# Kernel tuning notes

Measured on AMD Instinct MI355X. Metric: run time of the kernel, lower is better.

Reference implementation:

```python
import jax, jax.numpy as jnp
import numpy as np

NH, NKV, D = 16, 4, 64
E, NG, TKG, TOPK = 64, 8, 4, 8
RSF = 2.5
EPS = 1e-6
THETA = 10000.0

def rmsnorm(x, w, eps=EPS):
    v = jnp.mean(jnp.square(x.astype(jnp.float32)), axis=-1, keepdims=True)
    return (x * jax.lax.rsqrt(v + eps)).astype(x.dtype) * w

def rope_neox(x, pos):
    # x: [T, heads, D]; neox-style rotation over full head_dim
    d = x.shape[-1]
    inv = 1.0 / (THETA ** (jnp.arange(0, d, 2, dtype=jnp.float32) / d))
    f = pos.astype(jnp.float32)[:, None] * inv              # [T, d/2]
    cos = jnp.cos(f)[:, None, :]
    sin = jnp.sin(f)[:, None, :]
    x1, x2 = jnp.split(x, 2, axis=-1)
    return jnp.concatenate([x1 * cos - x2 * sin, x2 * cos + x1 * sin], axis=-1)


def setup_inputs() -> dict:
    key = jax.random.key(0)
    ks = jax.random.split(key, 12)
    T, H, I, IS = 2048, 1024, 256, 512
    s = 0.02
    return {
        "x": jax.random.normal(ks[0], (T, H), jnp.float32),
        "positions": jnp.arange(T, dtype=jnp.int32),
        "ln1_w": jnp.ones((H,), jnp.float32),
        "w_qkv": jax.random.normal(ks[1], (H, (NH + 2 * NKV) * D), jnp.float32) * s,
        "w_o": jax.random.normal(ks[2], (NH * D, H), jnp.float32) * s,
        "ln2_w": jnp.ones((H,), jnp.float32),
        "gate_w": jax.random.normal(ks[3], (E, H), jnp.float32) * s,
        "expert_bias": jax.random.normal(ks[4], (E,), jnp.float32) * 0.01,
        "we_gate": jax.random.normal(ks[5], (E, H, I), jnp.float32) * s,
        "we_up": jax.random.normal(ks[6], (E, H, I), jnp.float32) * s,
        "we_down": jax.random.normal(ks[7], (E, I, H), jnp.float32) * s,
        "ws_gate_up": jax.random.normal(ks[8], (H, 2 * IS), jnp.float32) * s,
        "ws_down": jax.random.normal(ks[9], (IS, H), jnp.float32) * s,
    }


def reference(x, positions, ln1_w, w_qkv, w_o, ln2_w, gate_w, expert_bias,
              we_gate, we_up, we_down, ws_gate_up, ws_down):
    T, H = x.shape
    residual = x
    # --- attention ---
    h = rmsnorm(x, ln1_w)
    qkv = h @ w_qkv
    q, k, v = jnp.split(qkv, [NH * D, (NH + NKV) * D], axis=-1)
    q = rope_neox(q.reshape(T, NH, D), positions)
    k = rope_neox(k.reshape(T, NKV, D), positions)
    v = v.reshape(T, NKV, D)
    rep = NH // NKV
    k = jnp.repeat(k, rep, axis=1)
    v = jnp.repeat(v, rep, axis=1)
    scores = jnp.einsum('thd,shd->hts', q, k) * (D ** -0.5)
    causal = positions[:, None] >= positions[None, :]
    scores = jnp.where(causal[None], scores, jnp.float32(-1e30))
    p = jax.nn.softmax(scores, axis=-1)
    attn = jnp.einsum('hts,shd->thd', p, v).reshape(T, NH * D)
    residual = residual + attn @ w_o
    # --- MoE block ---
    h = rmsnorm(residual, ln2_w)
    logits = h.astype(jnp.float32) @ gate_w.astype(jnp.float32).T      # [T,E]
    s = jax.nn.sigmoid(logits)
    sc = s + expert_bias[None, :]                                      # bias-corrected scores
    # grouped top-k: score each group by sum of its top-2 corrected scores
    gsc = sc.reshape(T, NG, E // NG)
    group_scores = jax.lax.top_k(gsc, 2)[0].sum(-1)                    # [T,NG]
    _, gidx = jax.lax.top_k(group_scores, TKG)
    gmask = jnp.zeros((T, NG), bool).at[jnp.arange(T)[:, None], gidx].set(True)
    sc_masked = jnp.where(jnp.repeat(gmask, E // NG, axis=1), sc, -jnp.inf)
    _, ids = jax.lax.top_k(sc_masked, TOPK)                            # [T,k]
    w = jnp.take_along_axis(s, ids, axis=-1)                           # weights from raw sigmoid scores
    w = w / (w.sum(-1, keepdims=True) + 1e-20)
    w = w * RSF
    combine = jnp.zeros((T, E), jnp.float32).at[jnp.arange(T)[:, None], ids].add(w)
    combine = combine.astype(h.dtype)
    # routed experts (dense-over-experts reference of the grouped-GEMM dispatch)
    g = jnp.einsum('th,ehi->tei', h, we_gate)
    u = jnp.einsum('th,ehi->tei', h, we_up)
    act = jax.nn.silu(g) * u
    y = jnp.einsum('tei,eih,te->th', act, we_down, combine)
    # shared expert (SwiGLU)
    gu = h @ ws_gate_up
    gs, us = jnp.split(gu, 2, axis=-1)
    y = y + (jax.nn.silu(gs) * us) @ ws_down
    return residual + y
```

## Files before the change

kernel.cpp:

```cpp
#include <hip/hip_runtime.h>
#include <hip/hip_bf16.h>
#include <math.h>

#define T_TOK 2048
#define H_DIM 1024
#define NHH 16
#define NKVH 4
#define HD 64
#define QKV_N 1536
#define NE 64
#define NGRP 8
#define TKG 4
#define TOPKK 8
#define EI 256
#define ISH 512
#define NPOS (T_TOK * TOPKK)

typedef __bf16 bf16_t;
typedef bf16_t bf16x8 __attribute__((ext_vector_type(8)));
typedef bf16_t bf16x4v __attribute__((ext_vector_type(4)));
typedef float f32x4 __attribute__((ext_vector_type(4)));

#define MFMA_BF16 __builtin_amdgcn_mfma_f32_16x16x32_bf16

__global__ void rmsnorm_k(const float* __restrict__ x, const float* __restrict__ w,
                          float* __restrict__ outf, bf16_t* __restrict__ outb) {
  const int t = blockIdx.x;
  const int tid = threadIdx.x;
  const float* xp = x + (size_t)t * H_DIM;
  const float4 x4 = *(const float4*)(xp + tid * 4);
  float s = x4.x * x4.x + x4.y * x4.y + x4.z * x4.z + x4.w * x4.w;
#pragma unroll
  for (int off = 32; off >= 1; off >>= 1) s += __shfl_xor(s, off);
  __shared__ float red[4];
  if ((tid & 63) == 0) red[tid >> 6] = s;
  __syncthreads();
  const float tot = red[0] + red[1] + red[2] + red[3];
  const float r = rsqrtf(tot / (float)H_DIM + 1e-6f);
  const float4 w4 = *(const float4*)(w + tid * 4);
  float4 o;
  o.x = x4.x * r * w4.x; o.y = x4.y * r * w4.y;
  o.z = x4.z * r * w4.z; o.w = x4.w * r * w4.w;
  if (outf) *(float4*)(outf + (size_t)t * H_DIM + tid * 4) = o;
  bf16x4v ob;
  ob[0] = (bf16_t)o.x; ob[1] = (bf16_t)o.y; ob[2] = (bf16_t)o.z; ob[3] = (bf16_t)o.w;
  *(bf16x4v*)(outb + (size_t)t * H_DIM + tid * 4) = ob;
}

__global__ void castT_k(const float* __restrict__ src, bf16_t* __restrict__ dst,
                        int R, int C, size_t srcStride, size_t dstStride,
                        int dstLD, int rowOff) {
  const int e = blockIdx.z;
  const float* sp = src + (size_t)e * srcStride;
  bf16_t* dp = dst + (size_t)e * dstStride;
  const int r0 = blockIdx.y * 32, c0 = blockIdx.x * 32;
  const int tid = threadIdx.x;
  __shared__ float tl[32][33];
  {
    const int rr = tid >> 3, cc4 = (tid & 7) * 4;
    const float4 v = *(const float4*)(sp + (size_t)(r0 + rr) * C + c0 + cc4);
    tl[rr][cc4 + 0] = v.x; tl[rr][cc4 + 1] = v.y;
    tl[rr][cc4 + 2] = v.z; tl[rr][cc4 + 3] = v.w;
  }
  __syncthreads();
  {
    const int cc = tid >> 3, rr4 = (tid & 7) * 4;
    bf16x4v o;
#pragma unroll
    for (int i = 0; i < 4; i++) o[i] = (bf16_t)tl[rr4 + i][cc];
    *(bf16x4v*)(dp + (size_t)(rowOff + c0 + cc) * dstLD + r0 + rr4) = o;
  }
}

__global__ __launch_bounds__(256) void mfma_gemm_k(
    const bf16_t* __restrict__ A, const bf16_t* __restrict__ Bt,
    const float* __restrict__ add0, const float* __restrict__ add1,
    float* __restrict__ C, int M, int N, int K) {
  __shared__ bf16_t Al[128 * 64];
  __shared__ bf16_t Bl[128 * 64];
  const int tid = threadIdx.x;
  const int lane = tid & 63, wave = tid >> 6;
  const int wm = wave >> 1, wn = wave & 1;
  const int lrow = lane & 15, lq = lane >> 4;
  const int m0 = blockIdx.y * 128, n0 = blockIdx.x * 128;
  const int arow = tid >> 1, qb = (tid & 1) * 4;
  const bf16_t* Arow = A + (size_t)(m0 + arow) * K + qb * 8;
  const bf16_t* Brow = Bt + (size_t)(n0 + arow) * K + qb * 8;
  f32x4 acc[4][4];
#pragma unroll
  for (int i = 0; i < 4; i++)
#pragma unroll
    for (int j = 0; j < 4; j++) acc[i][j] = (f32x4){0.f, 0.f, 0.f, 0.f};
  for (int k0 = 0; k0 < K; k0 += 64) {
    __syncthreads();
#pragma unroll
    for (int i = 0; i < 4; i++) {
      const int q = qb + i;
      *(bf16x8*)&Al[(q * 128 + arow) * 8] = *(const bf16x8*)(Arow + k0 + i * 8);
      *(bf16x8*)&Bl[(q * 128 + arow) * 8] = *(const bf16x8*)(Brow + k0 + i * 8);
    }
    __syncthreads();
#pragma unroll
    for (int kb = 0; kb < 2; kb++) {
      bf16x8 af[4], bfr[4];
#pragma unroll
      for (int i = 0; i < 4; i++) {
        af[i]  = *(const bf16x8*)&Al[((kb * 4 + lq) * 128 + wm * 64 + i * 16 + lrow) * 8];
        bfr[i] = *(const bf16x8*)&Bl[((kb * 4 + lq) * 128 + wn * 64 + i * 16 + lrow) * 8];
      }
#pragma unroll
      for (int i = 0; i < 4; i++)
#pragma unroll
        for (int j = 0; j < 4; j++)
          acc[i][j] = MFMA_BF16(af[i], bfr[j], acc[i][j], 0, 0, 0);
    }
  }
#pragma unroll
  for (int i = 0; i < 4; i++)
#pragma unroll
    for (int r = 0; r < 4; r++) {
      const int m = m0 + wm * 64 + i * 16 + lq * 4 + r;
#pragma unroll
      for (int j = 0; j < 4; j++) {
        const int n = n0 + wn * 64 + j * 16 + lrow;
        float v = acc[i][j][r];
        if (add0) v += add0[(size_t)m * N + n];
        if (add1) v += add1[(size_t)m * N + n];
        C[(size_t)m * N + n] = v;
      }
    }
}

__global__ __launch_bounds__(256) void mfma_gateup_k(
    const bf16_t* __restrict__ h2b, const bf16_t* __restrict__ weT,
    const int* __restrict__ ptok, const int* __restrict__ offs,
    bf16_t* __restrict__ gu_e) {
  const int e = blockIdx.z;
  const int base = offs[e];
  const int cnt = offs[e + 1] - base;
  const int m0 = blockIdx.y * 128;
  if (m0 >= cnt) return;
  const int n0 = blockIdx.x * 128;
  __shared__ bf16_t Al[128 * 64];
  __shared__ bf16_t Bl[128 * 64];
  __shared__ int toks[128];
  const int tid = threadIdx.x;
  if (tid < 128) toks[tid] = ptok[base + min(m0 + tid, cnt - 1)];
  const int lane = tid & 63, wave = tid >> 6;
  const int wm = wave >> 1, wn = wave & 1;
  const int lrow = lane & 15, lq = lane >> 4;
  const int arow = tid >> 1, qb = (tid & 1) * 4;
  const bf16_t* Bt = weT + (size_t)e * 512 * 1024;
  const bf16_t* Brow = Bt + (size_t)(n0 + arow) * 1024 + qb * 8;
  f32x4 acc[4][4];
#pragma unroll
  for (int i = 0; i < 4; i++)
#pragma unroll
    for (int j = 0; j < 4; j++) acc[i][j] = (f32x4){0.f, 0.f, 0.f, 0.f};
  for (int k0 = 0; k0 < 1024; k0 += 64) {
    __syncthreads();
    const bf16_t* Arow = h2b + (size_t)toks[arow] * 1024 + qb * 8;
#pragma unroll
    for (int i = 0; i < 4; i++) {
      const int q = qb + i;
      *(bf16x8*)&Al[(q * 128 + arow) * 8] = *(const bf16x8*)(Arow + k0 + i * 8);
      *(bf16x8*)&Bl[(q * 128 + arow) * 8] = *(const bf16x8*)(Brow + k0 + i * 8);
    }
    __syncthreads();
#pragma unroll
    for (int kb = 0; kb < 2; kb++) {
      bf16x8 af[4], bfr[4];
#pragma unroll
      for (int i = 0; i < 4; i++) {
        af[i]  = *(const bf16x8*)&Al[((kb * 4 + lq) * 128 + wm * 64 + i * 16 + lrow) * 8];
        bfr[i] = *(const bf16x8*)&Bl[((kb * 4 + lq) * 128 + wn * 64 + i * 16 + lrow) * 8];
      }
#pragma unroll
      for (int i = 0; i < 4; i++)
#pragma unroll
        for (int j = 0; j < 4; j++)
          acc[i][j] = MFMA_BF16(af[i], bfr[j], acc[i][j], 0, 0, 0);
    }
  }
#pragma unroll
  for (int i = 0; i < 4; i++)
#pragma unroll
    for (int r = 0; r < 4; r++) {
      const int mloc = m0 + wm * 64 + i * 16 + lq * 4 + r;
      if (mloc < cnt) {
#pragma unroll
        for (int j = 0; j < 4; j++) {
          const int n = n0 + wn * 64 + j * 16 + lrow;
          gu_e[(size_t)(base + mloc) * 512 + n] = (bf16_t)acc[i][j][r];
        }
      }
    }
}

__global__ __launch_bounds__(256) void mfma_down_k(
    const bf16_t* __restrict__ actb, const bf16_t* __restrict__ wdT,
    const int* __restrict__ ptok, const float* __restrict__ pw,
    const int* __restrict__ offs, float* __restrict__ y) {
  const int e = blockIdx.z;
  const int base = offs[e];
  const int cnt = offs[e + 1] - base;
  const int m0 = blockIdx.y * 128;
  if (m0 >= cnt) return;
  const int n0 = blockIdx.x * 128;
  __shared__ bf16_t Al[128 * 64];
  __shared__ bf16_t Bl[128 * 64];
  const int tid = threadIdx.x;
  const int lane = tid & 63, wave = tid >> 6;
  const int wm = wave >> 1, wn = wave & 1;
  const int lrow = lane & 15, lq = lane >> 4;
  const int arow = tid >> 1, qb = (tid & 1) * 4;
  const int agrow = base + min(m0 + arow, cnt - 1);
  const bf16_t* Arow = actb + (size_t)agrow * 256 + qb * 8;
  const bf16_t* Brow = wdT + (size_t)e * 1024 * 256 + (size_t)(n0 + arow) * 256 + qb * 8;
  f32x4 acc[4][4];
#pragma unroll
  for (int i = 0; i < 4; i++)
#pragma unroll
    for (int j = 0; j < 4; j++) acc[i][j] = (f32x4){0.f, 0.f, 0.f, 0.f};
  for (int k0 = 0; k0 < 256; k0 += 64) {
    __syncthreads();
#pragma unroll
    for (int i = 0; i < 4; i++) {
      const int q = qb + i;
      *(bf16x8*)&Al[(q * 128 + arow) * 8] = *(const bf16x8*)(Arow + k0 + i * 8);
      *(bf16x8*)&Bl[(q * 128 + arow) * 8] = *(const bf16x8*)(Brow + k0 + i * 8);
    }
    __syncthreads();
#pragma unroll
    for (int kb = 0; kb < 2; kb++) {
      bf16x8 af[4], bfr[4];
#pragma unroll
      for (int i = 0; i < 4; i++) {
        af[i]  = *(const bf16x8*)&Al[((kb * 4 + lq) * 128 + wm * 64 + i * 16 + lrow) * 8];
        bfr[i] = *(const bf16x8*)&Bl[((kb * 4 + lq) * 128 + wn * 64 + i * 16 + lrow) * 8];
      }
#pragma unroll
      for (int i = 0; i < 4; i++)
#pragma unroll
        for (int j = 0; j < 4; j++)
          acc[i][j] = MFMA_BF16(af[i], bfr[j], acc[i][j], 0, 0, 0);
    }
  }
#pragma unroll
  for (int i = 0; i < 4; i++)
#pragma unroll
    for (int r = 0; r < 4; r++) {
      const int mloc = m0 + wm * 64 + i * 16 + lq * 4 + r;
      if (mloc < cnt) {
        const float wv = pw[base + mloc];
        const int tok = ptok[base + mloc];
#pragma unroll
        for (int j = 0; j < 4; j++) {
          const int n = n0 + wn * 64 + j * 16 + lrow;
          atomicAdd(&y[(size_t)tok * H_DIM + n], wv * acc[i][j][r]);
        }
      }
    }
}

__global__ void rope_k(float* __restrict__ qkv, const int* __restrict__ positions) {
  const int t = blockIdx.x, h = blockIdx.y;
  const int i = threadIdx.x;
  const float inv = exp2f((float)i * (-13.287712379549449f / 32.0f));
  const float f = (float)positions[t] * inv;
  float sn, c;
  sincosf(f, &sn, &c);
  float* p = qkv + (size_t)t * QKV_N + h * HD;
  const float x1 = p[i], x2 = p[i + 32];
  p[i] = x1 * c - x2 * sn;
  p[i + 32] = x2 * c + x1 * sn;
}

__global__ __launch_bounds__(256) void attn_k(const float* __restrict__ qkv,
                                              bf16_t* __restrict__ attnb) {
  const int h = blockIdx.x;
  const int qt = (T_TOK / 64 - 1) - blockIdx.y;
  const int g = h >> 2;
  const int tid = threadIdx.x;
  const int lane = tid & 63, wave = tid >> 6;
  const int lcol = lane & 15, lk = lane >> 4;

  __shared__ bf16_t Kh[64][72];
  __shared__ bf16_t Ko[64][72];
  __shared__ bf16_t Vh[64][72];
  __shared__ bf16_t Vl[64][72];
  __shared__ bf16_t Ph[64][72];
  __shared__ bf16_t Po[64][72];

  bf16x8 aqh[2], aql[2];
  {
    const int qrow = qt * 64 + wave * 16 + lcol;
    const float* qp = qkv + (size_t)qrow * QKV_N + h * HD + lk * 8;
#pragma unroll
    for (int ks = 0; ks < 2; ks++) {
      const float4 a = *(const float4*)(qp + ks * 32);
      const float4 b = *(const float4*)(qp + ks * 32 + 4);
      const float qv[8] = {a.x, a.y, a.z, a.w, b.x, b.y, b.z, b.w};
#pragma unroll
      for (int j = 0; j < 8; j++) {
        const float v = qv[j] * 0.125f;
        const bf16_t hi = (bf16_t)v;
        aqh[ks][j] = hi;
        aql[ks][j] = (bf16_t)(v - (float)hi);
      }
    }
  }

  float m[4], l[4];
  f32x4 acc[4];
#pragma unroll
  for (int r = 0; r < 4; r++) { m[r] = -1e30f; l[r] = 0.f; }
#pragma unroll
  for (int n = 0; n < 4; n++) acc[n] = (f32x4){0.f, 0.f, 0.f, 0.f};

  const float* kbase = qkv + NHH * HD + g * HD;
  const float* vbase = qkv + (NHH + NKVH) * HD + g * HD;
  const int srow = tid >> 2;
  const int scb = tid & 3;

  for (int s0 = 0; s0 <= qt * 64; s0 += 64) {
    __syncthreads();
    {
      const float* kp = kbase + (size_t)(s0 + srow) * QKV_N + scb * 16;
      const float* vp = vbase + (size_t)(s0 + srow) * QKV_N + scb * 16;
      const float4 k0 = *(const float4*)(kp + 0);
      const float4 k1 = *(const float4*)(kp + 4);
      const float4 k2 = *(const float4*)(kp + 8);
      const float4 k3 = *(const float4*)(kp + 12);
      const float kv[16] = {k0.x, k0.y, k0.z, k0.w, k1.x, k1.y, k1.z, k1.w,
                            k2.x, k2.y, k2.z, k2.w, k3.x, k3.y, k3.z, k3.w};
      bf16x8 h0, h1, o0, o1;
#pragma unroll
      for (int j = 0; j < 8; j++) {
        const bf16_t hi = (bf16_t)kv[j];
        h0[j] = hi; o0[j] = (bf16_t)(kv[j] - (float)hi);
        const bf16_t hi2 = (bf16_t)kv[j + 8];
        h1[j] = hi2; o1[j] = (bf16_t)(kv[j + 8] - (float)hi2);
      }
      *(bf16x8*)&Kh[srow][scb * 16] = h0;
      *(bf16x8*)&Kh[srow][scb * 16 + 8] = h1;
      *(bf16x8*)&Ko[srow][scb * 16] = o0;
      *(bf16x8*)&Ko[srow][scb * 16 + 8] = o1;
      const float4 v0 = *(const float4*)(vp + 0);
      const float4 v1 = *(const float4*)(vp + 4);
      const float4 v2 = *(const float4*)(vp + 8);
      const float4 v3 = *(const float4*)(vp + 12);
      const float vv[16] = {v0.x, v0.y, v0.z, v0.w, v1.x, v1.y, v1.z, v1.w,
                            v2.x, v2.y, v2.z, v2.w, v3.x, v3.y, v3.z, v3.w};
#pragma unroll
      for (int r2 = 0; r2 < 16; r2++) {
        const int d = scb * 16 + r2;
        const int col = (srow + (d & 56)) & 63;
        const bf16_t hi = (bf16_t)vv[r2];
        Vh[d][col] = hi;
        Vl[d][col] = (bf16_t)(vv[r2] - (float)hi);
      }
    }
    __syncthreads();
    f32x4 s4[4];
#pragma unroll
    for (int n = 0; n < 4; n++) s4[n] = (f32x4){0.f, 0.f, 0.f, 0.f};
#pragma unroll
    for (int ks = 0; ks < 2; ks++) {
#pragma unroll
      for (int n = 0; n < 4; n++) {
        const bf16x8 bh = *(const bf16x8*)&Kh[n * 16 + lcol][ks * 32 + lk * 8];
        const bf16x8 bo = *(const bf16x8*)&Ko[n * 16 + lcol][ks * 32 + lk * 8];
        s4[n] = MFMA_BF16(aqh[ks], bh, s4[n], 0, 0, 0);
        s4[n] = MFMA_BF16(aqh[ks], bo, s4[n], 0, 0, 0);
        s4[n] = MFMA_BF16(aql[ks], bh, s4[n], 0, 0, 0);
      }
    }
    if (s0 == qt * 64) {
#pragma unroll
      for (int n = 0; n < 4; n++) {
        const int col = n * 16 + lcol;
#pragma unroll
        for (int r = 0; r < 4; r++)
          if (col > wave * 16 + lk * 4 + r) s4[n][r] = -1e30f;
      }
    }
#pragma unroll
    for (int r = 0; r < 4; r++) {
      float mx = fmaxf(fmaxf(s4[0][r], s4[1][r]), fmaxf(s4[2][r], s4[3][r]));
#pragma unroll
      for (int off = 1; off <= 8; off <<= 1) mx = fmaxf(mx, __shfl_xor(mx, off));
      const float mnew = fmaxf(m[r], mx);
      const float alpha = expf(m[r] - mnew);
      float ps = 0.f;
#pragma unroll
      for (int n = 0; n < 4; n++) {
        const float p = expf(s4[n][r] - mnew);
        s4[n][r] = p; ps += p;
      }
#pragma unroll
      for (int off = 1; off <= 8; off <<= 1) ps += __shfl_xor(ps, off);
      l[r] = l[r] * alpha + ps;
      m[r] = mnew;
#pragma unroll
      for (int n = 0; n < 4; n++) acc[n][r] *= alpha;
    }
#pragma unroll
    for (int n = 0; n < 4; n++)
#pragma unroll
      for (int r = 0; r < 4; r++) {
        const float p = s4[n][r];
        const bf16_t hi = (bf16_t)p;
        Ph[wave * 16 + lk * 4 + r][n * 16 + lcol] = hi;
        Po[wave * 16 + lk * 4 + r][n * 16 + lcol] = (bf16_t)(p - (float)hi);
      }
    __syncthreads();
#pragma unroll
    for (int ks = 0; ks < 2; ks++) {
      const bf16x8 pah = *(const bf16x8*)&Ph[wave * 16 + lcol][ks * 32 + lk * 8];
      const bf16x8 pao = *(const bf16x8*)&Po[wave * 16 + lcol][ks * 32 + lk * 8];
#pragma unroll
      for (int n = 0; n < 4; n++) {
        const int d = n * 16 + lcol;
        const int c0 = (ks * 32 + lk * 8 + (d & 56)) & 63;
        const bf16x8 bvh = *(const bf16x8*)&Vh[d][c0];
        const bf16x8 bvl = *(const bf16x8*)&Vl[d][c0];
        acc[n] = MFMA_BF16(pah, bvh, acc[n], 0, 0, 0);
        acc[n] = MFMA_BF16(pah, bvl, acc[n], 0, 0, 0);
        acc[n] = MFMA_BF16(pao, bvh, acc[n], 0, 0, 0);
      }
    }
  }
#pragma unroll
  for (int r = 0; r < 4; r++) {
    const int trow = qt * 64 + wave * 16 + lk * 4 + r;
    const float invl = 1.f / l[r];
#pragma unroll
    for (int n = 0; n < 4; n++)
      attnb[(size_t)trow * (NHH * HD) + h * HD + n * 16 + lcol] =
          (bf16_t)(acc[n][r] * invl);
  }
}

__global__ void gate_logits_k(const float* __restrict__ h2, const float* __restrict__ gw,
                              float* __restrict__ logits) {
  const int t = blockIdx.x;
  const int e = threadIdx.x;
  const float* hp = h2 + (size_t)t * H_DIM;
  const float* gp = gw + (size_t)e * H_DIM;
  float s = 0.f;
  for (int i = 0; i < H_DIM; i += 4) {
    const float4 h4 = *(const float4*)(hp + i);
    const float4 g4 = *(const float4*)(gp + i);
    s += h4.x * g4.x + h4.y * g4.y + h4.z * g4.z + h4.w * g4.w;
  }
  logits[t * NE + e] = s;
}

__global__ void route_k(const float* __restrict__ logits, const float* __restrict__ ebias,
                        int* __restrict__ topk_ids, float* __restrict__ topk_w) {
  const int t = blockIdx.x * 64 + threadIdx.x;
  if (t >= T_TOK) return;
  float s[NE], sc[NE];
  const float* lp = logits + t * NE;
#pragma unroll
  for (int e = 0; e < NE; e++) {
    const float v = 1.f / (1.f + expf(-lp[e]));
    s[e] = v;
    sc[e] = v + ebias[e];
  }
  float gsc[NGRP];
#pragma unroll
  for (int gi = 0; gi < NGRP; gi++) {
    float m1 = -1e30f, m2 = -1e30f;
#pragma unroll
    for (int j = 0; j < 8; j++) {
      const float v = sc[gi * 8 + j];
      if (v > m1) { m2 = m1; m1 = v; } else if (v > m2) m2 = v;
    }
    gsc[gi] = m1 + m2;
  }
  unsigned gmask = 0;
  for (int k2 = 0; k2 < TKG; k2++) {
    int bi = 0; float b = -3.4e38f;
#pragma unroll
    for (int gi = 0; gi < NGRP; gi++)
      if (!((gmask >> gi) & 1u) && gsc[gi] > b) { b = gsc[gi]; bi = gi; }
    gmask |= 1u << bi;
  }
  unsigned long long esel = 0ull;
  float wsum = 0.f;
  int ids[TOPKK]; float wv[TOPKK];
  for (int k2 = 0; k2 < TOPKK; k2++) {
    int bi = 0; float b = -3.4e38f;
    for (int e = 0; e < NE; e++) {
      if (((gmask >> (e >> 3)) & 1u) && !((esel >> e) & 1ull) && sc[e] > b) { b = sc[e]; bi = e; }
    }
    esel |= 1ull << bi;
    ids[k2] = bi;
    wv[k2] = s[bi];
    wsum += wv[k2];
  }
  const float norm = 2.5f / (wsum + 1e-20f);
#pragma unroll
  for (int k2 = 0; k2 < TOPKK; k2++) {
    topk_ids[t * TOPKK + k2] = ids[k2];
    topk_w[t * TOPKK + k2] = wv[k2] * norm;
  }
}

__global__ void count_k(const int* __restrict__ ids, int* __restrict__ counts) {
  const int idx = blockIdx.x * 256 + threadIdx.x;
  if (idx < NPOS) atomicAdd(&counts[ids[idx]], 1);
}

__global__ void offsets_k(const int* __restrict__ counts, int* __restrict__ offsets,
                          int* __restrict__ cursor) {
  if (threadIdx.x == 0 && blockIdx.x == 0) {
    int acc = 0;
    for (int e = 0; e < NE; e++) { offsets[e] = acc; cursor[e] = acc; acc += counts[e]; }
    offsets[NE] = acc;
  }
}

__global__ void scatter_k(const int* __restrict__ ids, const float* __restrict__ wts,
                          int* __restrict__ cursor, int* __restrict__ perm_tok,
                          float* __restrict__ perm_w) {
  const int idx = blockIdx.x * 256 + threadIdx.x;
  if (idx >= NPOS) return;
  const int e = ids[idx];
  const int pos = atomicAdd(&cursor[e], 1);
  perm_tok[pos] = idx >> 3;
  perm_w[pos] = wts[idx];
}

__global__ void act2_k(const bf16_t* __restrict__ gu_e, bf16_t* __restrict__ actb) {
  const int row = blockIdx.x;
  const int c = threadIdx.x;
  const float g = (float)gu_e[(size_t)row * 512 + c];
  const float u = (float)gu_e[(size_t)row * 512 + 256 + c];
  actb[(size_t)row * 256 + c] = (bf16_t)(g / (1.f + expf(-g)) * u);
}

__global__ void sact_k(const float* __restrict__ gu, bf16_t* __restrict__ sa) {
  const int idx = blockIdx.x * 256 + threadIdx.x;
  const int t = idx >> 9, i = idx & 511;
  const float g = gu[(size_t)t * 1024 + i];
  const float u = gu[(size_t)t * 1024 + 512 + i];
  sa[idx] = (bf16_t)(g / (1.f + expf(-g)) * u);
}

extern "C" void kernel_launch(void* const* d_in, const int* in_sizes, int n_in,
                              void* d_out, int out_size, void* d_ws, size_t ws_size,
                              hipStream_t stream) {
  const float* x         = (const float*)d_in[0];
  const int*   positions = (const int*)d_in[1];
  const float* ln1_w     = (const float*)d_in[2];
  const float* w_qkv     = (const float*)d_in[3];
  const float* w_o       = (const float*)d_in[4];
  const float* ln2_w     = (const float*)d_in[5];
  const float* gate_w    = (const float*)d_in[6];
  const float* ebias     = (const float*)d_in[7];
  const float* we_gate   = (const float*)d_in[8];
  const float* we_up     = (const float*)d_in[9];
  const float* we_down   = (const float*)d_in[10];
  const float* ws_gateup = (const float*)d_in[11];
  const float* ws_down   = (const float*)d_in[12];
  float* out = (float*)d_out;

  char* wsp = (char*)d_ws;
  size_t off = 0;
  auto alloc = [&](size_t bytes) {
    void* p = wsp + off;
    off += (bytes + 255) & ~(size_t)255;
    return p;
  };
  float*  qkv    = (float*)alloc((size_t)T_TOK * QKV_N * 4);
  bf16_t* attnb  = (bf16_t*)alloc((size_t)T_TOK * H_DIM * 2);
  bf16_t* gu_e   = (bf16_t*)qkv;
  bf16_t* h1b    = (bf16_t*)alloc((size_t)T_TOK * H_DIM * 2);
  bf16_t* sa     = h1b;
  float*  resid1 = (float*)alloc((size_t)T_TOK * H_DIM * 4);
  float*  h2f    = (float*)alloc((size_t)T_TOK * H_DIM * 4);
  bf16_t* h2b    = (bf16_t*)alloc((size_t)T_TOK * H_DIM * 2);
  float*  logits = (float*)alloc((size_t)T_TOK * NE * 4);
  int*    tids   = (int*)alloc((size_t)NPOS * 4);
  float*  tw     = (float*)alloc((size_t)NPOS * 4);
  int*    counts = (int*)alloc(NE * 4);
  int*    offs   = (int*)alloc((NE + 1) * 4);
  int*    cursor = (int*)alloc(NE * 4);
  int*    ptok   = (int*)alloc((size_t)NPOS * 4);
  float*  pw     = (float*)alloc((size_t)NPOS * 4);
  bf16_t* actb   = (bf16_t*)alloc((size_t)NPOS * EI * 2);
  float*  y      = (float*)alloc((size_t)T_TOK * H_DIM * 4);
  float*  gu     = (float*)alloc((size_t)T_TOK * 1024 * 4);
  bf16_t* wqkvT  = (bf16_t*)alloc((size_t)QKV_N * H_DIM * 2);
  bf16_t* woT    = (bf16_t*)alloc((size_t)H_DIM * H_DIM * 2);
  bf16_t* wsguT  = (bf16_t*)alloc((size_t)1024 * H_DIM * 2);
  bf16_t* wsdT   = (bf16_t*)alloc((size_t)H_DIM * ISH * 2);
  bf16_t* weT    = (bf16_t*)alloc((size_t)NE * 512 * H_DIM * 2);
  bf16_t* wdT    = (bf16_t*)alloc((size_t)NE * H_DIM * EI * 2);
  (void)ws_size; (void)in_sizes; (void)n_in; (void)out_size;

  castT_k<<<dim3(QKV_N / 32, H_DIM / 32, 1), 256, 0, stream>>>(
      w_qkv, wqkvT, H_DIM, QKV_N, 0, 0, H_DIM, 0);
  castT_k<<<dim3(H_DIM / 32, H_DIM / 32, 1), 256, 0, stream>>>(
      w_o, woT, H_DIM, H_DIM, 0, 0, H_DIM, 0);
  castT_k<<<dim3(1024 / 32, H_DIM / 32, 1), 256, 0, stream>>>(
      ws_gateup, wsguT, H_DIM, 1024, 0, 0, H_DIM, 0);
  castT_k<<<dim3(H_DIM / 32, ISH / 32, 1), 256, 0, stream>>>(
      ws_down, wsdT, ISH, H_DIM, 0, 0, ISH, 0);
  castT_k<<<dim3(EI / 32, H_DIM / 32, NE), 256, 0, stream>>>(
      we_gate, weT, H_DIM, EI, (size_t)H_DIM * EI, (size_t)512 * H_DIM, H_DIM, 0);
  castT_k<<<dim3(EI / 32, H_DIM / 32, NE), 256, 0, stream>>>(
      we_up, weT, H_DIM, EI, (size_t)H_DIM * EI, (size_t)512 * H_DIM, H_DIM, 256);
  castT_k<<<dim3(H_DIM / 32, EI / 32, NE), 256, 0, stream>>>(
      we_down, wdT, EI, H_DIM, (size_t)EI * H_DIM, (size_t)H_DIM * EI, EI, 0);

  hipMemsetAsync(counts, 0, NE * 4, stream);
  hipMemsetAsync(y, 0, (size_t)T_TOK * H_DIM * 4, stream);

  rmsnorm_k<<<T_TOK, 256, 0, stream>>>(x, ln1_w, nullptr, h1b);
  mfma_gemm_k<<<dim3(QKV_N / 128, T_TOK / 128), 256, 0, stream>>>(
      h1b, wqkvT, nullptr, nullptr, qkv, T_TOK, QKV_N, H_DIM);
  rope_k<<<dim3(T_TOK, NHH + NKVH), 32, 0, stream>>>(qkv, positions);
  attn_k<<<dim3(NHH, T_TOK / 64), 256, 0, stream>>>(qkv, attnb);
  mfma_gemm_k<<<dim3(H_DIM / 128, T_TOK / 128), 256, 0, stream>>>(
      attnb, woT, x, nullptr, resid1, T_TOK, H_DIM, H_DIM);

  rmsnorm_k<<<T_TOK, 256, 0, stream>>>(resid1, ln2_w, h2f, h2b);
  gate_logits_k<<<T_TOK, 64, 0, stream>>>(h2f, gate_w, logits);
  route_k<<<T_TOK / 64, 64, 0, stream>>>(logits, ebias, tids, tw);
  count_k<<<NPOS / 256, 256, 0, stream>>>(tids, counts);
  offsets_k<<<1, 1, 0, stream>>>(counts, offs, cursor);
  scatter_k<<<NPOS / 256, 256, 0, stream>>>(tids, tw, cursor, ptok, pw);

  mfma_gateup_k<<<dim3(512 / 128, T_TOK / 128, NE), 256, 0, stream>>>(
      h2b, weT, ptok, offs, gu_e);
  act2_k<<<NPOS, 256, 0, stream>>>(gu_e, actb);
  mfma_down_k<<<dim3(H_DIM / 128, T_TOK / 128, NE), 256, 0, stream>>>(
      actb, wdT, ptok, pw, offs, y);

  mfma_gemm_k<<<dim3(1024 / 128, T_TOK / 128), 256, 0, stream>>>(
      h2b, wsguT, nullptr, nullptr, gu, T_TOK, 1024, H_DIM);
  sact_k<<<(T_TOK * ISH) / 256, 256, 0, stream>>>(gu, sa);
  mfma_gemm_k<<<dim3(H_DIM / 128, T_TOK / 128), 256, 0, stream>>>(
      sa, wsdT, resid1, y, out, T_TOK, H_DIM, ISH);
}
```

Measured before the change: 827.6 us.

## Use direct global-to-LDS loads with XOR swizzle in GEMMs; precompute split K/V

```diff
diff --git a/kernel.cpp b/kernel.cpp
--- a/kernel.cpp
+++ b/kernel.cpp
@@ -22,6 +22,11 @@
 typedef float f32x4 __attribute__((ext_vector_type(4)));
 
 #define MFMA_BF16 __builtin_amdgcn_mfma_f32_16x16x32_bf16
+
+#define GLOAD16(gsrc, ldst)                                            \
+  __builtin_amdgcn_global_load_lds(                                    \
+      (const __attribute__((address_space(1))) void*)(gsrc),           \
+      (__attribute__((address_space(3))) void*)(ldst), 16, 0, 0)
 
 __global__ void rmsnorm_k(const float* __restrict__ x, const float* __restrict__ w,
                           float* __restrict__ outf, bf16_t* __restrict__ outb) {
@@ -72,6 +77,7 @@
   }
 }
 
+
 __global__ __launch_bounds__(256) void mfma_gemm_k(
     const bf16_t* __restrict__ A, const bf16_t* __restrict__ Bt,
     const float* __restrict__ add0, const float* __restrict__ add1,
@@ -83,9 +89,6 @@
   const int wm = wave >> 1, wn = wave & 1;
   const int lrow = lane & 15, lq = lane >> 4;
   const int m0 = blockIdx.y * 128, n0 = blockIdx.x * 128;
-  const int arow = tid >> 1, qb = (tid & 1) * 4;
-  const bf16_t* Arow = A + (size_t)(m0 + arow) * K + qb * 8;
-  const bf16_t* Brow = Bt + (size_t)(n0 + arow) * K + qb * 8;
   f32x4 acc[4][4];
 #pragma unroll
   for (int i = 0; i < 4; i++)
@@ -95,18 +98,23 @@
     __syncthreads();
 #pragma unroll
     for (int i = 0; i < 4; i++) {
-      const int q = qb + i;
-      *(bf16x8*)&Al[(q * 128 + arow) * 8] = *(const bf16x8*)(Arow + k0 + i * 8);
-      *(bf16x8*)&Bl[(q * 128 + arow) * 8] = *(const bf16x8*)(Brow + k0 + i * 8);
+      const int j = wave * 4 + i;
+      const int rowl = j * 8 + (lane >> 3);
+      const int q = (lane & 7) ^ ((rowl >> 1) & 7);
+      GLOAD16(A + (size_t)(m0 + rowl) * K + k0 + q * 8, &Al[j * 512]);
+      GLOAD16(Bt + (size_t)(n0 + rowl) * K + k0 + q * 8, &Bl[j * 512]);
     }
     __syncthreads();
 #pragma unroll
     for (int kb = 0; kb < 2; kb++) {
+      const int qq = kb * 4 + lq;
       bf16x8 af[4], bfr[4];
 #pragma unroll
       for (int i = 0; i < 4; i++) {
-        af[i]  = *(const bf16x8*)&Al[((kb * 4 + lq) * 128 + wm * 64 + i * 16 + lrow) * 8];
-        bfr[i] = *(const bf16x8*)&Bl[((kb * 4 + lq) * 128 + wn * 64 + i * 16 + lrow) * 8];
+        const int ra = wm * 64 + i * 16 + lrow;
+        const int rb = wn * 64 + i * 16 + lrow;
+        af[i]  = *(const bf16x8*)&Al[(ra * 8 + (qq ^ ((ra >> 1) & 7))) * 8];
+        bfr[i] = *(const bf16x8*)&Bl[(rb * 8 + (qq ^ ((rb >> 1) & 7))) * 8];
       }
 #pragma unroll
       for (int i = 0; i < 4; i++)
@@ -149,9 +157,7 @@
   const int lane = tid & 63, wave = tid >> 6;
   const int wm = wave >> 1, wn = wave & 1;
   const int lrow = lane & 15, lq = lane >> 4;
-  const int arow = tid >> 1, qb = (tid & 1) * 4;
-  const bf16_t* Bt = weT + (size_t)e * 512 * 1024;
-  const bf16_t* Brow = Bt + (size_t)(n0 + arow) * 1024 + qb * 8;
+  const bf16_t* Bt = weT + (size_t)e * 512 * 1024 + (size_t)n0 * 1024;
   f32x4 acc[4][4];
 #pragma unroll
   for (int i = 0; i < 4; i++)
@@ -159,21 +165,25 @@
     for (int j = 0; j < 4; j++) acc[i][j] = (f32x4){0.f, 0.f, 0.f, 0.f};
   for (int k0 = 0; k0 < 1024; k0 += 64) {
     __syncthreads();
-    const bf16_t* Arow = h2b + (size_t)toks[arow] * 1024 + qb * 8;
 #pragma unroll
     for (int i = 0; i < 4; i++) {
-      const int q = qb + i;
-      *(bf16x8*)&Al[(q * 128 + arow) * 8] = *(const bf16x8*)(Arow + k0 + i * 8);
-      *(bf16x8*)&Bl[(q * 128 + arow) * 8] = *(const bf16x8*)(Brow + k0 + i * 8);
+      const int j = wave * 4 + i;
+      const int rowl = j * 8 + (lane >> 3);
+      const int q = (lane & 7) ^ ((rowl >> 1) & 7);
+      GLOAD16(h2b + (size_t)toks[rowl] * 1024 + k0 + q * 8, &Al[j * 512]);
+      GLOAD16(Bt + (size_t)rowl * 1024 + k0 + q * 8, &Bl[j * 512]);
     }
     __syncthreads();
 #pragma unroll
     for (int kb = 0; kb < 2; kb++) {
+      const int qq = kb * 4 + lq;
       bf16x8 af[4], bfr[4];
 #pragma unroll
       for (int i = 0; i < 4; i++) {
-        af[i]  = *(const bf16x8*)&Al[((kb * 4 + lq) * 128 + wm * 64 + i * 16 + lrow) * 8];
-        bfr[i] = *(const bf16x8*)&Bl[((kb * 4 + lq) * 128 + wn * 64 + i * 16 + lrow) * 8];
+        const int ra = wm * 64 + i * 16 + lrow;
+        const int rb = wn * 64 + i * 16 + lrow;
+        af[i]  = *(const bf16x8*)&Al[(ra * 8 + (qq ^ ((ra >> 1) & 7))) * 8];
+        bfr[i] = *(const bf16x8*)&Bl[(rb * 8 + (qq ^ ((rb >> 1) & 7))) * 8];
       }
 #pragma unroll
       for (int i = 0; i < 4; i++)
@@ -213,10 +223,7 @@
   const int lane = tid & 63, wave = tid >> 6;
   const int wm = wave >> 1, wn = wave & 1;
   const int lrow = lane & 15, lq = lane >> 4;
-  const int arow = tid >> 1, qb = (tid & 1) * 4;
-  const int agrow = base + min(m0 + arow, cnt - 1);
-  const bf16_t* Arow = actb + (size_t)agrow * 256 + qb * 8;
-  const bf16_t* Brow = wdT + (size_t)e * 1024 * 256 + (size_t)(n0 + arow) * 256 + qb * 8;
+  const bf16_t* Bt = wdT + (size_t)e * 1024 * 256 + (size_t)n0 * 256;
   f32x4 acc[4][4];
 #pragma unroll
   for (int i = 0; i < 4; i++)
@@ -226,18 +233,24 @@
     __syncthreads();
 #pragma unroll
     for (int i = 0; i < 4; i++) {
-      const int q = qb + i;
-      *(bf16x8*)&Al[(q * 128 + arow) * 8] = *(const bf16x8*)(Arow + k0 + i * 8);
-      *(bf16x8*)&Bl[(q * 128 + arow) * 8] = *(const bf16x8*)(Brow + k0 + i * 8);
+      const int j = wave * 4 + i;
+      const int rowl = j * 8 + (lane >> 3);
+      const int q = (lane & 7) ^ ((rowl >> 1) & 7);
+      const int aRow = base + min(m0 + rowl, cnt - 1);
+      GLOAD16(actb + (size_t)aRow * 256 + k0 + q * 8, &Al[j * 512]);
+      GLOAD16(Bt + (size_t)rowl * 256 + k0 + q * 8, &Bl[j * 512]);
     }
     __syncthreads();
 #pragma unroll
     for (int kb = 0; kb < 2; kb++) {
+      const int qq = kb * 4 + lq;
       bf16x8 af[4], bfr[4];
 #pragma unroll
       for (int i = 0; i < 4; i++) {
-        af[i]  = *(const bf16x8*)&Al[((kb * 4 + lq) * 128 + wm * 64 + i * 16 + lrow) * 8];
-        bfr[i] = *(const bf16x8*)&Bl[((kb * 4 + lq) * 128 + wn * 64 + i * 16 + lrow) * 8];
+        const int ra = wm * 64 + i * 16 + lrow;
+        const int rb = wn * 64 + i * 16 + lrow;
+        af[i]  = *(const bf16x8*)&Al[(ra * 8 + (qq ^ ((ra >> 1) & 7))) * 8];
+        bfr[i] = *(const bf16x8*)&Bl[(rb * 8 + (qq ^ ((rb >> 1) & 7))) * 8];
       }
 #pragma unroll
       for (int i = 0; i < 4; i++)
@@ -276,8 +289,67 @@
   p[i + 32] = x2 * c + x1 * sn;
 }
 
-__global__ __launch_bounds__(256) void attn_k(const float* __restrict__ qkv,
-                                              bf16_t* __restrict__ attnb) {
+__global__ __launch_bounds__(256) void kvprep_k(
+    const float* __restrict__ qkv, bf16_t* __restrict__ kh, bf16_t* __restrict__ kl,
+    bf16_t* __restrict__ vh, bf16_t* __restrict__ vl) {
+  const int tile = blockIdx.x, g = blockIdx.y;
+  const int tid = threadIdx.x;
+  const int srow = tid >> 2, scb = tid & 3;
+  const int t = tile * 64 + srow;
+  const float* kp = qkv + (size_t)t * QKV_N + NHH * HD + g * HD + scb * 16;
+  const float* vp = kp + NKVH * HD;
+  __shared__ bf16_t Vsh[64][72];
+  __shared__ bf16_t Vsl[64][72];
+  {
+    const float4 k0 = *(const float4*)(kp + 0);
+    const float4 k1 = *(const float4*)(kp + 4);
+    const float4 k2 = *(const float4*)(kp + 8);
+    const float4 k3 = *(const float4*)(kp + 12);
+    const float kv[16] = {k0.x, k0.y, k0.z, k0.w, k1.x, k1.y, k1.z, k1.w,
+                          k2.x, k2.y, k2.z, k2.w, k3.x, k3.y, k3.z, k3.w};
+    bf16x8 h0, h1, o0, o1;
+#pragma unroll
+    for (int j = 0; j < 8; j++) {
+      const bf16_t hi = (bf16_t)kv[j];
+      h0[j] = hi; o0[j] = (bf16_t)(kv[j] - (float)hi);
+      const bf16_t hi2 = (bf16_t)kv[j + 8];
+      h1[j] = hi2; o1[j] = (bf16_t)(kv[j + 8] - (float)hi2);
+    }
+    bf16_t* khp = kh + ((size_t)g * T_TOK + t) * 64 + scb * 16;
+    bf16_t* klp = kl + ((size_t)g * T_TOK + t) * 64 + scb * 16;
+    *(bf16x8*)(khp) = h0; *(bf16x8*)(khp + 8) = h1;
+    *(bf16x8*)(klp) = o0; *(bf16x8*)(klp + 8) = o1;
+  }
+  {
+    const float4 v0 = *(const float4*)(vp + 0);
+    const float4 v1 = *(const float4*)(vp + 4);
+    const float4 v2 = *(const float4*)(vp + 8);
+    const float4 v3 = *(const float4*)(vp + 12);
+    const float vv[16] = {v0.x, v0.y, v0.z, v0.w, v1.x, v1.y, v1.z, v1.w,
+                          v2.x, v2.y, v2.z, v2.w, v3.x, v3.y, v3.z, v3.w};
+#pragma unroll
+    for (int r2 = 0; r2 < 16; r2++) {
+      const int d = scb * 16 + r2;
+      const int col = (srow + (d & 56)) & 63;
+      const bf16_t hi = (bf16_t)vv[r2];
+      Vsh[d][col] = hi;
+      Vsl[d][col] = (bf16_t)(vv[r2] - (float)hi);
+    }
+  }
+  __syncthreads();
+  {
+    const size_t ob = (((size_t)g * (T_TOK / 64) + tile) * 64 + srow) * 64 + scb * 16;
+    *(bf16x8*)(vh + ob)     = *(const bf16x8*)&Vsh[srow][scb * 16];
+    *(bf16x8*)(vh + ob + 8) = *(const bf16x8*)&Vsh[srow][scb * 16 + 8];
+    *(bf16x8*)(vl + ob)     = *(const bf16x8*)&Vsl[srow][scb * 16];
+    *(bf16x8*)(vl + ob + 8) = *(const bf16x8*)&Vsl[srow][scb * 16 + 8];
+  }
+}
+
+__global__ __launch_bounds__(256) void attn_k(
+    const float* __restrict__ qkv, const bf16_t* __restrict__ kh_g,
+    const bf16_t* __restrict__ kl_g, const bf16_t* __restrict__ vh_g,
+    const bf16_t* __restrict__ vl_g, bf16_t* __restrict__ attnb) {
   const int h = blockIdx.x;
   const int qt = (T_TOK / 64 - 1) - blockIdx.y;
   const int g = h >> 2;
@@ -318,48 +390,26 @@
 #pragma unroll
   for (int n = 0; n < 4; n++) acc[n] = (f32x4){0.f, 0.f, 0.f, 0.f};
 
-  const float* kbase = qkv + NHH * HD + g * HD;
-  const float* vbase = qkv + (NHH + NKVH) * HD + g * HD;
+  const bf16_t* khB = kh_g + (size_t)g * T_TOK * 64;
+  const bf16_t* klB = kl_g + (size_t)g * T_TOK * 64;
+  const bf16_t* vhB = vh_g + (size_t)g * (T_TOK / 64) * 64 * 64;
+  const bf16_t* vlB = vl_g + (size_t)g * (T_TOK / 64) * 64 * 64;
   const int srow = tid >> 2;
   const int scb = tid & 3;
 
   for (int s0 = 0; s0 <= qt * 64; s0 += 64) {
     __syncthreads();
     {
-      const float* kp = kbase + (size_t)(s0 + srow) * QKV_N + scb * 16;
-      const float* vp = vbase + (size_t)(s0 + srow) * QKV_N + scb * 16;
-      const float4 k0 = *(const float4*)(kp + 0);
-      const float4 k1 = *(const float4*)(kp + 4);
-      const float4 k2 = *(const float4*)(kp + 8);
-      const float4 k3 = *(const float4*)(kp + 12);
-      const float kv[16] = {k0.x, k0.y, k0.z, k0.w, k1.x, k1.y, k1.z, k1.w,
-                            k2.x, k2.y, k2.z, k2.w, k3.x, k3.y, k3.z, k3.w};
-      bf16x8 h0, h1, o0, o1;
-#pragma unroll
-      for (int j = 0; j < 8; j++) {
-        const bf16_t hi = (bf16_t)kv[j];
-        h0[j] = hi; o0[j] = (bf16_t)(kv[j] - (float)hi);
-        const bf16_t hi2 = (bf16_t)kv[j + 8];
-        h1[j] = hi2; o1[j] = (bf16_t)(kv[j + 8] - (float)hi2);
-      }
-      *(bf16x8*)&Kh[srow][scb * 16] = h0;
-      *(bf16x8*)&Kh[srow][scb * 16 + 8] = h1;
-      *(bf16x8*)&Ko[srow][scb * 16] = o0;
-      *(bf16x8*)&Ko[srow][scb * 16 + 8] = o1;
-      const float4 v0 = *(const float4*)(vp + 0);
-      const float4 v1 = *(const float4*)(vp + 4);
-      const float4 v2 = *(const float4*)(vp + 8);
-      const float4 v3 = *(const float4*)(vp + 12);
-      const float vv[16] = {v0.x, v0.y, v0.z, v0.w, v1.x, v1.y, v1.z, v1.w,
-                            v2.x, v2.y, v2.z, v2.w, v3.x, v3.y, v3.z, v3.w};
-#pragma unroll
-      for (int r2 = 0; r2 < 16; r2++) {
-        const int d = scb * 16 + r2;
-        const int col = (srow + (d & 56)) & 63;
-        const bf16_t hi = (bf16_t)vv[r2];
-        Vh[d][col] = hi;
-        Vl[d][col] = (bf16_t)(vv[r2] - (float)hi);
-      }
+      const size_t kb0 = (size_t)(s0 + srow) * 64 + scb * 16;
+      *(bf16x8*)&Kh[srow][scb * 16]     = *(const bf16x8*)(khB + kb0);
+      *(bf16x8*)&Kh[srow][scb * 16 + 8] = *(const bf16x8*)(khB + kb0 + 8);
+      *(bf16x8*)&Ko[srow][scb * 16]     = *(const bf16x8*)(klB + kb0);
+      *(bf16x8*)&Ko[srow][scb * 16 + 8] = *(const bf16x8*)(klB + kb0 + 8);
+      const size_t vb0 = ((size_t)(s0 >> 6) * 64 + srow) * 64 + scb * 16;
+      *(bf16x8*)&Vh[srow][scb * 16]     = *(const bf16x8*)(vhB + vb0);
+      *(bf16x8*)&Vh[srow][scb * 16 + 8] = *(const bf16x8*)(vhB + vb0 + 8);
+      *(bf16x8*)&Vl[srow][scb * 16]     = *(const bf16x8*)(vlB + vb0);
+      *(bf16x8*)&Vl[srow][scb * 16 + 8] = *(const bf16x8*)(vlB + vb0 + 8);
     }
     __syncthreads();
     f32x4 s4[4];
@@ -600,6 +650,10 @@
   bf16_t* wsdT   = (bf16_t*)alloc((size_t)H_DIM * ISH * 2);
   bf16_t* weT    = (bf16_t*)alloc((size_t)NE * 512 * H_DIM * 2);
   bf16_t* wdT    = (bf16_t*)alloc((size_t)NE * H_DIM * EI * 2);
+  bf16_t* kvkh   = (bf16_t*)alloc((size_t)NKVH * T_TOK * 64 * 2);
+  bf16_t* kvkl   = (bf16_t*)alloc((size_t)NKVH * T_TOK * 64 * 2);
+  bf16_t* kvvh   = (bf16_t*)alloc((size_t)NKVH * T_TOK * 64 * 2);
+  bf16_t* kvvl   = (bf16_t*)alloc((size_t)NKVH * T_TOK * 64 * 2);
   (void)ws_size; (void)in_sizes; (void)n_in; (void)out_size;
 
   castT_k<<<dim3(QKV_N / 32, H_DIM / 32, 1), 256, 0, stream>>>(
@@ -624,7 +678,8 @@
   mfma_gemm_k<<<dim3(QKV_N / 128, T_TOK / 128), 256, 0, stream>>>(
       h1b, wqkvT, nullptr, nullptr, qkv, T_TOK, QKV_N, H_DIM);
   rope_k<<<dim3(T_TOK, NHH + NKVH), 32, 0, stream>>>(qkv, positions);
-  attn_k<<<dim3(NHH, T_TOK / 64), 256, 0, stream>>>(qkv, attnb);
+  kvprep_k<<<dim3(T_TOK / 64, NKVH), 256, 0, stream>>>(qkv, kvkh, kvkl, kvvh, kvvl);
+  attn_k<<<dim3(NHH, T_TOK / 64), 256, 0, stream>>>(qkv, kvkh, kvkl, kvvh, kvvl, attnb);
   mfma_gemm_k<<<dim3(H_DIM / 128, T_TOK / 128), 256, 0, stream>>>(
       attnb, woT, x, nullptr, resid1, T_TOK, H_DIM, H_DIM);
 
```

After: 816.2 us. No clear change (-1.4%).
